# Performance work log

Measured on AMD Instinct MI355X. Metric: run time of the kernel, lower is better.

Reference implementation:

```python
import jax, jax.numpy as jnp
import numpy as np

N, E, F, H = 50000, 800000, 64, 4
NEG_SLOPE = 0.2
LN_EPS = 1e-5


def setup_inputs() -> dict:
    key = jax.random.key(0)
    ks = jax.random.split(key, 12)
    h = jax.random.normal(ks[0], (N, F), dtype=jnp.float32)
    src = jax.random.randint(ks[1], (E,), 0, N, dtype=jnp.int32)
    dst = jax.random.randint(ks[2], (E,), 0, N, dtype=jnp.int32)
    s = 1.0 / np.sqrt(F)
    fc_w = jax.random.uniform(ks[3], (F, H * F), jnp.float32, -s, s)
    attn_l = jax.random.normal(ks[4], (H, F), dtype=jnp.float32) * s
    attn_r = jax.random.normal(ks[5], (H, F), dtype=jnp.float32) * s
    gat_bias = jnp.zeros((H * F,), dtype=jnp.float32)
    so = 1.0 / np.sqrt(H * F)
    out_w = jax.random.uniform(ks[6], (H * F, F), jnp.float32, -so, so)
    out_b = jax.random.uniform(ks[7], (F,), jnp.float32, -so, so)
    ln_g = jnp.ones((F,), dtype=jnp.float32)
    ln_b = jnp.zeros((F,), dtype=jnp.float32)
    return {"h": h, "src": src, "dst": dst, "fc_w": fc_w, "attn_l": attn_l,
            "attn_r": attn_r, "gat_bias": gat_bias, "out_w": out_w,
            "out_b": out_b, "ln_g": ln_g, "ln_b": ln_b}


def reference(h, src, dst, fc_w, attn_l, attn_r, gat_bias, out_w, out_b, ln_g, ln_b):
    # --- GATConv (DGL semantics) ---
    feat = (h @ fc_w).reshape(N, H, F)                      # [N,H,F]
    el = jnp.einsum('nhf,hf->nh', feat, attn_l)             # [N,H]
    er = jnp.einsum('nhf,hf->nh', feat, attn_r)             # [N,H]
    e = jax.nn.leaky_relu(el[src] + er[dst], NEG_SLOPE)     # [E,H]
    # edge softmax over incoming edges of each dst node
    m = jax.ops.segment_max(e, dst, num_segments=N)         # [N,H]
    ex = jnp.exp(e - m[dst])                                # [E,H]
    z = jax.ops.segment_sum(ex, dst, num_segments=N)        # [N,H]
    alpha = ex / z[dst]                                     # [E,H]
    msg = feat[src] * alpha[:, :, None]                     # [E,H,F]
    rst = jax.ops.segment_sum(msg, dst, num_segments=N)     # [N,H,F]
    rst = rst + gat_bias.reshape(H, F)
    # --- out linear + layernorm ---
    x = rst.reshape(N, H * F) @ out_w + out_b               # [N,F]
    mu = jnp.mean(x, axis=-1, keepdims=True)
    var = jnp.var(x, axis=-1, keepdims=True)
    return (x - mu) * jax.lax.rsqrt(var + LN_EPS) * ln_g + ln_b
```

## Files before the change

### kernel.cpp

```cpp
#include <hip/hip_runtime.h>

#define NN 50000
#define EE 800000
#define FF 64
#define HH 4
#define HF 256
#define NEG_SLOPE 0.2f
#define LN_EPS 1e-5f
#define WPACK_N (4 * 8 * 64 * 8)
#define WPACKA_N (16 * 2 * 64 * 8)
#define NTILE (NN / 16)
#define TROW 264

typedef __attribute__((ext_vector_type(8))) short s8v;
typedef __attribute__((ext_vector_type(4))) float f4v;

__device__ __forceinline__ unsigned short f32_to_bf16_rne(float x) {
  unsigned int u = __float_as_uint(x);
  unsigned int r = u + 0x7FFFu + ((u >> 16) & 1u);
  return (unsigned short)(r >> 16);
}

__global__ __launch_bounds__(256) void k_prep(
    const float* __restrict__ fc_w, const float* __restrict__ out_w,
    unsigned short* __restrict__ wpackA, unsigned short* __restrict__ wpack,
    int* __restrict__ cnt) {
  const int idx = blockIdx.x * 256 + threadIdx.x;
  if (idx < WPACKA_N) {
    const int j = idx & 7;
    const int l = (idx >> 3) & 63;
    const int t = (idx >> 9) & 1;
    const int ct = idx >> 10;
    const int k = 32 * t + (l >> 4) * 8 + j;
    const int c = 16 * ct + (l & 15);
    wpackA[idx] = f32_to_bf16_rne(fc_w[k * HF + c]);
  } else if (idx < WPACKA_N + WPACK_N) {
    const int i2 = idx - WPACKA_N;
    const int j = i2 & 7;
    const int l = (i2 >> 3) & 63;
    const int t = (i2 >> 9) & 7;
    const int ct = i2 >> 12;
    const int k = 32 * t + (l >> 4) * 8 + j;
    const int c = 16 * ct + (l & 15);
    wpack[i2] = f32_to_bf16_rne(out_w[k * FF + c]);
  }
  if (idx < NN) cnt[idx] = 0;
}

__global__ __launch_bounds__(256) void k_feat(
    const float* __restrict__ h, const unsigned short* __restrict__ wpackA,
    const float* __restrict__ attn_l, const float* __restrict__ attn_r,
    unsigned short* __restrict__ featb, float* __restrict__ el,
    float* __restrict__ er) {
  __shared__ unsigned short wlds[WPACKA_N];
  {
    const uint4* s = (const uint4*)wpackA;
    uint4* d = (uint4*)wlds;
    for (int i = threadIdx.x; i < 2048; i += 256) d[i] = s[i];
  }
  __syncthreads();
  const int wave = threadIdx.x >> 6;
  const int lane = threadIdx.x & 63;
  const int tile = blockIdx.x * 4 + wave;
  if (tile >= NTILE) return;
  const int n0 = tile * 16;
  const int cl = lane & 15;
  const int quad = lane >> 4;

  float al[16], ar[16];
#pragma unroll
  for (int ct = 0; ct < 16; ++ct) {
    al[ct] = attn_l[16 * ct + cl];
    ar[ct] = attn_r[16 * ct + cl];
  }

  s8v a[2];
#pragma unroll
  for (int t = 0; t < 2; ++t) {
    const float* hp = h + (size_t)(n0 + cl) * FF + 32 * t + quad * 8;
    float hv[8];
    *(float4*)hv = *(const float4*)hp;
    *(float4*)(hv + 4) = *(const float4*)(hp + 4);
    s8v av;
#pragma unroll
    for (int i = 0; i < 8; ++i) av[i] = (short)f32_to_bf16_rne(hv[i]);
    a[t] = av;
  }

  f4v acc[16];
#pragma unroll
  for (int ct = 0; ct < 16; ++ct) {
    f4v z = {0.f, 0.f, 0.f, 0.f};
    acc[ct] = z;
#pragma unroll
    for (int t = 0; t < 2; ++t) {
      const s8v b = *(const s8v*)(wlds + ((ct * 2 + t) * 64 + lane) * 8);
      acc[ct] = __builtin_amdgcn_mfma_f32_16x16x32_bf16(a[t], b, acc[ct], 0, 0, 0);
    }
  }

#pragma unroll
  for (int r = 0; r < 4; ++r) {
    const int n = n0 + quad * 4 + r;
    float pl[4] = {0.f, 0.f, 0.f, 0.f};
    float pr[4] = {0.f, 0.f, 0.f, 0.f};
#pragma unroll
    for (int g = 0; g < 4; ++g) {
      const float x0 = acc[g][r];
      const float x1 = acc[g + 4][r];
      const float x2 = acc[g + 8][r];
      const float x3 = acc[g + 12][r];
      uint2 pk;
      pk.x = (unsigned)f32_to_bf16_rne(x0) | ((unsigned)f32_to_bf16_rne(x1) << 16);
      pk.y = (unsigned)f32_to_bf16_rne(x2) | ((unsigned)f32_to_bf16_rne(x3) << 16);
      *(uint2*)(featb + (size_t)n * HF + (16 * g + cl) * 4) = pk;
      pl[0] = fmaf(x0, al[g], pl[0]);      pr[0] = fmaf(x0, ar[g], pr[0]);
      pl[1] = fmaf(x1, al[g + 4], pl[1]);  pr[1] = fmaf(x1, ar[g + 4], pr[1]);
      pl[2] = fmaf(x2, al[g + 8], pl[2]);  pr[2] = fmaf(x2, ar[g + 8], pr[2]);
      pl[3] = fmaf(x3, al[g + 12], pl[3]); pr[3] = fmaf(x3, ar[g + 12], pr[3]);
    }
#pragma unroll
    for (int off = 1; off < 16; off <<= 1) {
#pragma unroll
      for (int hh = 0; hh < 4; ++hh) {
        pl[hh] += __shfl_xor(pl[hh], off, 64);
        pr[hh] += __shfl_xor(pr[hh], off, 64);
      }
    }
    if (cl == 0) {
      *(float4*)(el + (size_t)n * 4) = make_float4(pl[0], pl[1], pl[2], pl[3]);
      *(float4*)(er + (size_t)n * 4) = make_float4(pr[0], pr[1], pr[2], pr[3]);
    }
  }
}

__global__ void k_scatter(const int* __restrict__ src,
                          const int* __restrict__ dst,
                          int* __restrict__ cnt, int* __restrict__ colp) {
  int e = blockIdx.x * blockDim.x + threadIdx.x;
  if (e < EE) {
    const int d = dst[e];
    const int pos = atomicAdd(&cnt[d], 1);
    if (pos < 64) colp[(d << 6) | pos] = src[e];
  }
}

__global__ __launch_bounds__(256) void k_gather_out(
    const unsigned short* __restrict__ featb, const float* __restrict__ el,
    const float* __restrict__ er, const int* __restrict__ cnt,
    const int* __restrict__ colp, const float* __restrict__ gat_bias,
    const unsigned short* __restrict__ wpack, const float* __restrict__ out_b,
    const float* __restrict__ ln_g, const float* __restrict__ ln_b,
    float* __restrict__ out) {
  __shared__ unsigned short tile[16][TROW];
  __shared__ float part[4][16][2];
  __shared__ float wtab[4][64][4];
  const int wave = threadIdx.x >> 6;
  const int lane = threadIdx.x & 63;
  const int n0 = blockIdx.x * 16;
  const float gb0 = gat_bias[lane], gb1 = gat_bias[64 + lane];
  const float gb2 = gat_bias[128 + lane], gb3 = gat_bias[192 + lane];
  const unsigned short* fb = featb + lane * HH;

#pragma unroll
  for (int r = 0; r < 4; ++r) {
    const int row = wave * 4 + r;
    const int n = n0 + row;
    int mm = cnt[n];
    mm = mm > 64 ? 64 : mm;
    const int m = __builtin_amdgcn_readfirstlane(mm);
    const float4 erv = *(const float4*)(er + (size_t)n * 4);
    int s = 0;
    float w0 = 0.f, w1 = 0.f, w2 = 0.f, w3 = 0.f;
    if (lane < m) {
      s = colp[(n << 6) | lane];
      const float4 elv = *(const float4*)(el + (size_t)s * 4);
      float e0 = elv.x + erv.x, e1 = elv.y + erv.y;
      float e2 = elv.z + erv.z, e3 = elv.w + erv.w;
      e0 = e0 > 0.f ? e0 : NEG_SLOPE * e0;
      e1 = e1 > 0.f ? e1 : NEG_SLOPE * e1;
      e2 = e2 > 0.f ? e2 : NEG_SLOPE * e2;
      e3 = e3 > 0.f ? e3 : NEG_SLOPE * e3;
      w0 = __expf(e0); w1 = __expf(e1);
      w2 = __expf(e2); w3 = __expf(e3);
    }
    float z0 = w0, z1 = w1, z2 = w2, z3 = w3;
#pragma unroll
    for (int off = 1; off < 64; off <<= 1) {
      z0 += __shfl_xor(z0, off, 64);
      z1 += __shfl_xor(z1, off, 64);
      z2 += __shfl_xor(z2, off, 64);
      z3 += __shfl_xor(z3, off, 64);
    }
    const float zi0 = z0 > 0.f ? 1.f / z0 : 0.f;
    const float zi1 = z1 > 0.f ? 1.f / z1 : 0.f;
    const float zi2 = z2 > 0.f ? 1.f / z2 : 0.f;
    const float zi3 = z3 > 0.f ? 1.f / z3 : 0.f;
    w0 *= zi0; w1 *= zi1; w2 *= zi2; w3 *= zi3;
    *(float4*)&wtab[wave][lane][0] = make_float4(w0, w1, w2, w3);

    float a0 = 0.f, a1 = 0.f, a2 = 0.f, a3 = 0.f;
    for (int e = 0; e < m; e += 8) {
#pragma unroll
      for (int j = 0; j < 8; ++j) {
        const int le = e + j;
        const int se = __builtin_amdgcn_readlane(s, le);
        const uint2 d = *(const uint2*)(fb + (size_t)se * HF);
        const float4 w = *(const float4*)&wtab[wave][le][0];
        a0 = fmaf(w.x, __uint_as_float(d.x << 16), a0);
        a1 = fmaf(w.y, __uint_as_float(d.x & 0xFFFF0000u), a1);
        a2 = fmaf(w.z, __uint_as_float(d.y << 16), a2);
        a3 = fmaf(w.w, __uint_as_float(d.y & 0xFFFF0000u), a3);
      }
    }
    tile[row][lane]       = f32_to_bf16_rne(a0 + gb0);
    tile[row][64 + lane]  = f32_to_bf16_rne(a1 + gb1);
    tile[row][128 + lane] = f32_to_bf16_rne(a2 + gb2);
    tile[row][192 + lane] = f32_to_bf16_rne(a3 + gb3);
  }
  __syncthreads();

  const int cl = lane & 15;
  const int quad = lane >> 4;
  s8v afr[8];
#pragma unroll
  for (int t = 0; t < 8; ++t)
    afr[t] = *(const s8v*)(&tile[cl][32 * t + quad * 8]);

  f4v acc = {0.f, 0.f, 0.f, 0.f};
#pragma unroll
  for (int t = 0; t < 8; ++t) {
    const s8v b = *(const s8v*)(wpack + ((wave * 8 + t) * 64 + lane) * 8);
    acc = __builtin_amdgcn_mfma_f32_16x16x32_bf16(afr[t], b, acc, 0, 0, 0);
  }

  const float ob = out_b[16 * wave + cl];
  float xv[4];
#pragma unroll
  for (int r = 0; r < 4; ++r) {
    const float v = acc[r] + ob;
    xv[r] = v;
    float p1 = v, p2 = v * v;
#pragma unroll
    for (int off = 1; off < 16; off <<= 1) {
      p1 += __shfl_xor(p1, off, 64);
      p2 += __shfl_xor(p2, off, 64);
    }
    if (cl == 0) {
      part[wave][quad * 4 + r][0] = p1;
      part[wave][quad * 4 + r][1] = p2;
    }
  }
  __syncthreads();
#pragma unroll
  for (int r = 0; r < 4; ++r) {
    const int row = quad * 4 + r;
    const float t1 = part[0][row][0] + part[1][row][0] +
                     part[2][row][0] + part[3][row][0];
    const float t2 = part[0][row][1] + part[1][row][1] +
                     part[2][row][1] + part[3][row][1];
    const float mu = t1 * (1.f / 64.f);
    const float var = t2 * (1.f / 64.f) - mu * mu;
    const float inv = rsqrtf(var + LN_EPS);
    const int c = 16 * wave + cl;
    out[(size_t)(n0 + row) * FF + c] = (xv[r] - mu) * inv * ln_g[c] + ln_b[c];
  }
}

extern "C" void kernel_launch(void* const* d_in, const int* in_sizes, int n_in,
                              void* d_out, int out_size, void* d_ws,
                              size_t ws_size, hipStream_t stream) {
  const float* h_in   = (const float*)d_in[0];
  const int*   src    = (const int*)d_in[1];
  const int*   dst    = (const int*)d_in[2];
  const float* fc_w   = (const float*)d_in[3];
  const float* attn_l = (const float*)d_in[4];
  const float* attn_r = (const float*)d_in[5];
  const float* gbias  = (const float*)d_in[6];
  const float* out_w  = (const float*)d_in[7];
  const float* out_b  = (const float*)d_in[8];
  const float* ln_g   = (const float*)d_in[9];
  const float* ln_b   = (const float*)d_in[10];
  float* out = (float*)d_out;

  char* p = (char*)d_ws;
  auto alloc = [&](size_t bytes) {
    char* q = p;
    p += (bytes + 255) & ~(size_t)255;
    return q;
  };
  unsigned short* featb  = (unsigned short*)alloc((size_t)NN * HF * 2);
  unsigned short* wpack  = (unsigned short*)alloc((size_t)WPACK_N * 2);
  unsigned short* wpackA = (unsigned short*)alloc((size_t)WPACKA_N * 2);
  float* el      = (float*)alloc((size_t)NN * HH * 4);
  float* er      = (float*)alloc((size_t)NN * HH * 4);
  int*   cnt     = (int*)alloc((size_t)NN * 4);
  int*   colp    = (int*)alloc((size_t)NN * 64 * 4);

  k_prep<<<256, 256, 0, stream>>>(fc_w, out_w, wpackA, wpack, cnt);
  k_feat<<<(NTILE + 3) / 4, 256, 0, stream>>>(h_in, wpackA, attn_l, attn_r,
                                              featb, el, er);
  k_scatter<<<(EE + 255) / 256, 256, 0, stream>>>(src, dst, cnt, colp);
  k_gather_out<<<NTILE, 256, 0, stream>>>(featb, el, er, cnt, colp, gbias,
                                          wpack, out_b, ln_g, ln_b, out);
}
```

Measured before the change: 215.0 us.

## Fuse feat and scatter kernels, persistent gather with atomic tile queue

Merges the feature-projection and edge-scatter kernels into one launch, with blocks partitioned by index. The feat path now reads the packed weights straight from global memory instead of staging them in LDS. The gather kernel becomes persistent: a fixed grid of blocks pulls 16-node tiles from an atomic counter. Softmax normalization is folded into the gather loop by broadcasting the edge weights with readlane and dividing once at the end, which drops the wave-wide shuffle reduction and the LDS weight table. These cut launch count, shuffle and LDS traffic, and tail imbalance, at the cost of atomic queue contention and more scalar readlane work per edge.

```diff
diff --git a/kernel.cpp b/kernel.cpp
--- a/kernel.cpp
+++ b/kernel.cpp
@@ -11,6 +11,9 @@
 #define WPACKA_N (16 * 2 * 64 * 8)
 #define NTILE (NN / 16)
 #define TROW 264
+#define FEAT_BLOCKS ((NTILE + 3) / 4)
+#define SCAT_BLOCKS ((EE + 255) / 256)
+#define GATHER_BLOCKS 2048
 
 typedef __attribute__((ext_vector_type(8))) short s8v;
 typedef __attribute__((ext_vector_type(4))) float f4v;
@@ -21,10 +24,15 @@
   return (unsigned short)(r >> 16);
 }
 
+__device__ __forceinline__ float readlane_f(float v, int l) {
+  return __uint_as_float(
+      (unsigned)__builtin_amdgcn_readlane((int)__float_as_uint(v), l));
+}
+
 __global__ __launch_bounds__(256) void k_prep(
     const float* __restrict__ fc_w, const float* __restrict__ out_w,
     unsigned short* __restrict__ wpackA, unsigned short* __restrict__ wpack,
-    int* __restrict__ cnt) {
+    int* __restrict__ cnt, int* __restrict__ tnext) {
   const int idx = blockIdx.x * 256 + threadIdx.x;
   if (idx < WPACKA_N) {
     const int j = idx & 7;
@@ -45,23 +53,29 @@
     wpack[i2] = f32_to_bf16_rne(out_w[k * FF + c]);
   }
   if (idx < NN) cnt[idx] = 0;
-}
-
-__global__ __launch_bounds__(256) void k_feat(
+  if (idx == 0) *tnext = 0;
+}
+
+__global__ __launch_bounds__(256) void k_feat_scatter(
     const float* __restrict__ h, const unsigned short* __restrict__ wpackA,
     const float* __restrict__ attn_l, const float* __restrict__ attn_r,
     unsigned short* __restrict__ featb, float* __restrict__ el,
-    float* __restrict__ er) {
-  __shared__ unsigned short wlds[WPACKA_N];
-  {
-    const uint4* s = (const uint4*)wpackA;
-    uint4* d = (uint4*)wlds;
-    for (int i = threadIdx.x; i < 2048; i += 256) d[i] = s[i];
-  }
-  __syncthreads();
+    float* __restrict__ er, const int* __restrict__ src,
+    const int* __restrict__ dst, int* __restrict__ cnt,
+    int* __restrict__ colp) {
+  const int bid = blockIdx.x;
+  if (bid >= FEAT_BLOCKS) {
+    const int e = (bid - FEAT_BLOCKS) * 256 + threadIdx.x;
+    if (e < EE) {
+      const int d = dst[e];
+      const int pos = atomicAdd(&cnt[d], 1);
+      if (pos < 64) colp[(d << 6) | pos] = src[e];
+    }
+    return;
+  }
   const int wave = threadIdx.x >> 6;
   const int lane = threadIdx.x & 63;
-  const int tile = blockIdx.x * 4 + wave;
+  const int tile = bid * 4 + wave;
   if (tile >= NTILE) return;
   const int n0 = tile * 16;
   const int cl = lane & 15;
@@ -94,7 +108,7 @@
     acc[ct] = z;
 #pragma unroll
     for (int t = 0; t < 2; ++t) {
-      const s8v b = *(const s8v*)(wlds + ((ct * 2 + t) * 64 + lane) * 8);
+      const s8v b = *(const s8v*)(wpackA + ((ct * 2 + t) * 64 + lane) * 8);
       acc[ct] = __builtin_amdgcn_mfma_f32_16x16x32_bf16(a[t], b, acc[ct], 0, 0, 0);
     }
   }
@@ -134,136 +148,124 @@
   }
 }
 
-__global__ void k_scatter(const int* __restrict__ src,
-                          const int* __restrict__ dst,
-                          int* __restrict__ cnt, int* __restrict__ colp) {
-  int e = blockIdx.x * blockDim.x + threadIdx.x;
-  if (e < EE) {
-    const int d = dst[e];
-    const int pos = atomicAdd(&cnt[d], 1);
-    if (pos < 64) colp[(d << 6) | pos] = src[e];
-  }
-}
-
 __global__ __launch_bounds__(256) void k_gather_out(
     const unsigned short* __restrict__ featb, const float* __restrict__ el,
     const float* __restrict__ er, const int* __restrict__ cnt,
     const int* __restrict__ colp, const float* __restrict__ gat_bias,
     const unsigned short* __restrict__ wpack, const float* __restrict__ out_b,
     const float* __restrict__ ln_g, const float* __restrict__ ln_b,
-    float* __restrict__ out) {
+    int* __restrict__ tnext, float* __restrict__ out) {
   __shared__ unsigned short tile[16][TROW];
   __shared__ float part[4][16][2];
-  __shared__ float wtab[4][64][4];
+  __shared__ int tsh;
   const int wave = threadIdx.x >> 6;
   const int lane = threadIdx.x & 63;
-  const int n0 = blockIdx.x * 16;
+  const int cl = lane & 15;
+  const int quad = lane >> 4;
   const float gb0 = gat_bias[lane], gb1 = gat_bias[64 + lane];
   const float gb2 = gat_bias[128 + lane], gb3 = gat_bias[192 + lane];
   const unsigned short* fb = featb + lane * HH;
-
-#pragma unroll
-  for (int r = 0; r < 4; ++r) {
-    const int row = wave * 4 + r;
-    const int n = n0 + row;
-    int mm = cnt[n];
-    mm = mm > 64 ? 64 : mm;
-    const int m = __builtin_amdgcn_readfirstlane(mm);
-    const float4 erv = *(const float4*)(er + (size_t)n * 4);
-    int s = 0;
-    float w0 = 0.f, w1 = 0.f, w2 = 0.f, w3 = 0.f;
-    if (lane < m) {
-      s = colp[(n << 6) | lane];
-      const float4 elv = *(const float4*)(el + (size_t)s * 4);
-      float e0 = elv.x + erv.x, e1 = elv.y + erv.y;
-      float e2 = elv.z + erv.z, e3 = elv.w + erv.w;
-      e0 = e0 > 0.f ? e0 : NEG_SLOPE * e0;
-      e1 = e1 > 0.f ? e1 : NEG_SLOPE * e1;
-      e2 = e2 > 0.f ? e2 : NEG_SLOPE * e2;
-      e3 = e3 > 0.f ? e3 : NEG_SLOPE * e3;
-      w0 = __expf(e0); w1 = __expf(e1);
-      w2 = __expf(e2); w3 = __expf(e3);
-    }
-    float z0 = w0, z1 = w1, z2 = w2, z3 = w3;
-#pragma unroll
-    for (int off = 1; off < 64; off <<= 1) {
-      z0 += __shfl_xor(z0, off, 64);
-      z1 += __shfl_xor(z1, off, 64);
-      z2 += __shfl_xor(z2, off, 64);
-      z3 += __shfl_xor(z3, off, 64);
-    }
-    const float zi0 = z0 > 0.f ? 1.f / z0 : 0.f;
-    const float zi1 = z1 > 0.f ? 1.f / z1 : 0.f;
-    const float zi2 = z2 > 0.f ? 1.f / z2 : 0.f;
-    const float zi3 = z3 > 0.f ? 1.f / z3 : 0.f;
-    w0 *= zi0; w1 *= zi1; w2 *= zi2; w3 *= zi3;
-    *(float4*)&wtab[wave][lane][0] = make_float4(w0, w1, w2, w3);
-
-    float a0 = 0.f, a1 = 0.f, a2 = 0.f, a3 = 0.f;
-    for (int e = 0; e < m; e += 8) {
-#pragma unroll
-      for (int j = 0; j < 8; ++j) {
-        const int le = e + j;
-        const int se = __builtin_amdgcn_readlane(s, le);
-        const uint2 d = *(const uint2*)(fb + (size_t)se * HF);
-        const float4 w = *(const float4*)&wtab[wave][le][0];
-        a0 = fmaf(w.x, __uint_as_float(d.x << 16), a0);
-        a1 = fmaf(w.y, __uint_as_float(d.x & 0xFFFF0000u), a1);
-        a2 = fmaf(w.z, __uint_as_float(d.y << 16), a2);
-        a3 = fmaf(w.w, __uint_as_float(d.y & 0xFFFF0000u), a3);
-      }
-    }
-    tile[row][lane]       = f32_to_bf16_rne(a0 + gb0);
-    tile[row][64 + lane]  = f32_to_bf16_rne(a1 + gb1);
-    tile[row][128 + lane] = f32_to_bf16_rne(a2 + gb2);
-    tile[row][192 + lane] = f32_to_bf16_rne(a3 + gb3);
-  }
-  __syncthreads();
-
-  const int cl = lane & 15;
-  const int quad = lane >> 4;
-  s8v afr[8];
-#pragma unroll
-  for (int t = 0; t < 8; ++t)
-    afr[t] = *(const s8v*)(&tile[cl][32 * t + quad * 8]);
-
-  f4v acc = {0.f, 0.f, 0.f, 0.f};
-#pragma unroll
-  for (int t = 0; t < 8; ++t) {
-    const s8v b = *(const s8v*)(wpack + ((wave * 8 + t) * 64 + lane) * 8);
-    acc = __builtin_amdgcn_mfma_f32_16x16x32_bf16(afr[t], b, acc, 0, 0, 0);
-  }
-
   const float ob = out_b[16 * wave + cl];
-  float xv[4];
-#pragma unroll
-  for (int r = 0; r < 4; ++r) {
-    const float v = acc[r] + ob;
-    xv[r] = v;
-    float p1 = v, p2 = v * v;
-#pragma unroll
-    for (int off = 1; off < 16; off <<= 1) {
-      p1 += __shfl_xor(p1, off, 64);
-      p2 += __shfl_xor(p2, off, 64);
-    }
-    if (cl == 0) {
-      part[wave][quad * 4 + r][0] = p1;
-      part[wave][quad * 4 + r][1] = p2;
-    }
-  }
-  __syncthreads();
-#pragma unroll
-  for (int r = 0; r < 4; ++r) {
-    const int row = quad * 4 + r;
-    const float t1 = part[0][row][0] + part[1][row][0] +
-                     part[2][row][0] + part[3][row][0];
-    const float t2 = part[0][row][1] + part[1][row][1] +
-                     part[2][row][1] + part[3][row][1];
-    const float mu = t1 * (1.f / 64.f);
-    const float var = t2 * (1.f / 64.f) - mu * mu;
-    const float inv = rsqrtf(var + LN_EPS);
-    const int c = 16 * wave + cl;
-    out[(size_t)(n0 + row) * FF + c] = (xv[r] - mu) * inv * ln_g[c] + ln_b[c];
+  const float lg = ln_g[16 * wave + cl];
+  const float lb = ln_b[16 * wave + cl];
+
+  for (;;) {
+    if (threadIdx.x == 0) tsh = atomicAdd(tnext, 1);
+    __syncthreads();
+    const int t = tsh;
+    if (t >= NTILE) break;
+    const int n0 = t * 16;
+
+#pragma unroll
+    for (int r = 0; r < 4; ++r) {
+      const int row = wave * 4 + r;
+      const int n = n0 + row;
+      int mm = cnt[n];
+      mm = mm > 64 ? 64 : mm;
+      const int m = __builtin_amdgcn_readfirstlane(mm);
+      const float4 erv = *(const float4*)(er + (size_t)n * 4);
+      int s = 0;
+      float a0 = 0.f, a1 = 0.f, a2 = 0.f, a3 = 0.f;
+      float z0 = 0.f, z1 = 0.f, z2 = 0.f, z3 = 0.f;
+      float w0 = 0.f, w1 = 0.f, w2 = 0.f, w3 = 0.f;
+      if (lane < m) {
+        s = colp[(n << 6) | lane];
+        const float4 elv = *(const float4*)(el + (size_t)s * 4);
+        float e0 = elv.x + erv.x, e1 = elv.y + erv.y;
+        float e2 = elv.z + erv.z, e3 = elv.w + erv.w;
+        e0 = e0 > 0.f ? e0 : NEG_SLOPE * e0;
+        e1 = e1 > 0.f ? e1 : NEG_SLOPE * e1;
+        e2 = e2 > 0.f ? e2 : NEG_SLOPE * e2;
+        e3 = e3 > 0.f ? e3 : NEG_SLOPE * e3;
+        w0 = __expf(e0); w1 = __expf(e1);
+        w2 = __expf(e2); w3 = __expf(e3);
+      }
+      for (int e = 0; e < m; e += 8) {
+#pragma unroll
+        for (int j = 0; j < 8; ++j) {
+          const int le = e + j;
+          const int se = __builtin_amdgcn_readlane(s, le);
+          const float we0 = readlane_f(w0, le);
+          const float we1 = readlane_f(w1, le);
+          const float we2 = readlane_f(w2, le);
+          const float we3 = readlane_f(w3, le);
+          const uint2 d = *(const uint2*)(fb + (size_t)se * HF);
+          z0 += we0; z1 += we1; z2 += we2; z3 += we3;
+          a0 = fmaf(we0, __uint_as_float(d.x << 16), a0);
+          a1 = fmaf(we1, __uint_as_float(d.x & 0xFFFF0000u), a1);
+          a2 = fmaf(we2, __uint_as_float(d.y << 16), a2);
+          a3 = fmaf(we3, __uint_as_float(d.y & 0xFFFF0000u), a3);
+        }
+      }
+      tile[row][lane]       = f32_to_bf16_rne((z0 > 0.f ? a0 / z0 : 0.f) + gb0);
+      tile[row][64 + lane]  = f32_to_bf16_rne((z1 > 0.f ? a1 / z1 : 0.f) + gb1);
+      tile[row][128 + lane] = f32_to_bf16_rne((z2 > 0.f ? a2 / z2 : 0.f) + gb2);
+      tile[row][192 + lane] = f32_to_bf16_rne((z3 > 0.f ? a3 / z3 : 0.f) + gb3);
+    }
+    __syncthreads();
+
+    s8v afr[8];
+#pragma unroll
+    for (int t8 = 0; t8 < 8; ++t8)
+      afr[t8] = *(const s8v*)(&tile[cl][32 * t8 + quad * 8]);
+
+    f4v acc = {0.f, 0.f, 0.f, 0.f};
+#pragma unroll
+    for (int t8 = 0; t8 < 8; ++t8) {
+      const s8v b = *(const s8v*)(wpack + ((wave * 8 + t8) * 64 + lane) * 8);
+      acc = __builtin_amdgcn_mfma_f32_16x16x32_bf16(afr[t8], b, acc, 0, 0, 0);
+    }
+
+    float xv[4];
+#pragma unroll
+    for (int r = 0; r < 4; ++r) {
+      const float v = acc[r] + ob;
+      xv[r] = v;
+      float p1 = v, p2 = v * v;
+#pragma unroll
+      for (int off = 1; off < 16; off <<= 1) {
+        p1 += __shfl_xor(p1, off, 64);
+        p2 += __shfl_xor(p2, off, 64);
+      }
+      if (cl == 0) {
+        part[wave][quad * 4 + r][0] = p1;
+        part[wave][quad * 4 + r][1] = p2;
+      }
+    }
+    __syncthreads();
+#pragma unroll
+    for (int r = 0; r < 4; ++r) {
+      const int row = quad * 4 + r;
+      const float t1 = part[0][row][0] + part[1][row][0] +
+                       part[2][row][0] + part[3][row][0];
+      const float t2 = part[0][row][1] + part[1][row][1] +
+                       part[2][row][1] + part[3][row][1];
+      const float mu = t1 * (1.f / 64.f);
+      const float var = t2 * (1.f / 64.f) - mu * mu;
+      const float inv = rsqrtf(var + LN_EPS);
+      out[(size_t)(n0 + row) * FF + 16 * wave + cl] =
+          (xv[r] - mu) * inv * lg + lb;
+    }
   }
 }
 
@@ -296,11 +298,12 @@
   float* er      = (float*)alloc((size_t)NN * HH * 4);
   int*   cnt     = (int*)alloc((size_t)NN * 4);
   int*   colp    = (int*)alloc((size_t)NN * 64 * 4);
-
-  k_prep<<<256, 256, 0, stream>>>(fc_w, out_w, wpackA, wpack, cnt);
-  k_feat<<<(NTILE + 3) / 4, 256, 0, stream>>>(h_in, wpackA, attn_l, attn_r,
-                                              featb, el, er);
-  k_scatter<<<(EE + 255) / 256, 256, 0, stream>>>(src, dst, cnt, colp);
-  k_gather_out<<<NTILE, 256, 0, stream>>>(featb, el, er, cnt, colp, gbias,
-                                          wpack, out_b, ln_g, ln_b, out);
-}
+  int*   tnext   = (int*)alloc(256);
+
+  k_prep<<<256, 256, 0, stream>>>(fc_w, out_w, wpackA, wpack, cnt, tnext);
+  k_feat_scatter<<<FEAT_BLOCKS + SCAT_BLOCKS, 256, 0, stream>>>(
+      h_in, wpackA, attn_l, attn_r, featb, el, er, src, dst, cnt, colp);
+  k_gather_out<<<GATHER_BLOCKS, 256, 0, stream>>>(featb, el, er, cnt, colp,
+                                                  gbias, wpack, out_b, ln_g,
+                                                  ln_b, tnext, out);
+}
```

New measurement: 255.4 us. 18.8% more time.
